# Kernel tuning notes

Measured on AMD Instinct MI355X. Metric: run time of the kernel, lower is better.

The kernel has to match this reference:

```python
import jax, jax.numpy as jnp
import numpy as np

N_HEADS = 4


def setup_inputs() -> dict:
    key = jax.random.key(0)
    ks = jax.random.split(key, 8)
    T, B, V, F = 30, 64, 32, 128   # len_pred, batch, n_vehicles, feature_size
    L, LF, TH = 64, 64, 20         # n_lanes, lane_feature_size, len_hist
    vehicles = jax.random.normal(ks[0], (T, B, V, F), dtype=jnp.float32)
    lanes = jax.random.normal(ks[1], (B, V, L, LF), dtype=jnp.float32)
    mask_lanes = jax.random.randint(ks[2], (TH, B, V, L), 0, 2).astype(bool)
    # torch Linear weight layout [out, in]; conv 1x1 weights squeezed to [out, in]
    Wk = jax.random.normal(ks[3], (F, LF), dtype=jnp.float32) / np.sqrt(LF)
    Wv = jax.random.normal(ks[4], (F, LF), dtype=jnp.float32) / np.sqrt(LF)
    Wq = jax.random.normal(ks[5], (F, F), dtype=jnp.float32) / np.sqrt(F)
    Wc = jax.random.normal(ks[6], (F, F), dtype=jnp.float32) / np.sqrt(F)
    return {"vehicles": vehicles, "lanes": lanes, "mask_lanes": mask_lanes,
            "Wk": Wk, "Wv": Wv, "Wq": Wq, "Wc": Wc}


def reference(vehicles, lanes, mask_lanes, Wk, Wv, Wq, Wc):
    # vehicles: [T,B,V,F], lanes: [B,V,L,LF], mask_lanes: [TH,B,V,L] bool
    T, B, V, F = vehicles.shape
    L = lanes.shape[2]
    H = N_HEADS
    hd = F // H
    # Linear projections of lanes (torch Linear: y = x @ W.T)
    k = jnp.einsum('bvlf,gf->bvlg', lanes, Wk).reshape(B, V, L, H, hd)
    v = jnp.einsum('bvlf,gf->bvlg', lanes, Wv).reshape(B, V, L, H, hd)
    # 1x1 Conv2d on feature channels == per-position linear
    q = jnp.einsum('tbvf,gf->tbvg', vehicles, Wq).reshape(T, B, V, H, hd)
    # mask: any over history dim -> [B,V,L] (the second any in attention is a no-op
    # since the mask is repeated identically over T and heads)
    mask = jnp.any(mask_lanes, axis=0)  # [B,V,L]
    scores = jnp.einsum('tbvhd,bvlhd->tbvhl', q, k) / jnp.sqrt(jnp.float32(hd))
    scores = jnp.where(mask[None, :, :, None, :], scores, jnp.float32(-1e9))
    p = jax.nn.softmax(scores, axis=-1)  # [T,B,V,H,L]
    out = jnp.einsum('tbvhl,bvlhd->tbvhd', p, v).reshape(T, B, V, F)
    out = jnp.einsum('tbvf,gf->tbvg', out, Wc) + vehicles
    return out
```

## Files before the change

### kernel.cpp

```cpp
#include <hip/hip_runtime.h>
#include <hip/hip_bf16.h>

#define T_  30
#define B_  64
#define V_  32
#define F_  128
#define L_  64
#define LF_ 64
#define TH_ 20
#define H_  4
#define HD_ 32

typedef __attribute__((ext_vector_type(8))) short bf16x8;
typedef __attribute__((ext_vector_type(4))) float f32x4;
#define MFMA(a,b,c) __builtin_amdgcn_mfma_f32_16x16x32_bf16(a, b, c, 0, 0, 0)

__device__ __forceinline__ float bf1(unsigned short u) {
    unsigned int x = ((unsigned int)u) << 16; float f; __builtin_memcpy(&f, &x, 4); return f;
}
__device__ __forceinline__ unsigned int cvtpk(float a, float b) {
    __hip_bfloat162 h = __float22bfloat162_rn(make_float2(a, b));
    unsigned int r; __builtin_memcpy(&r, &h, 4); return r;
}
__device__ __forceinline__ void st4pk(unsigned short* p, float a, float b, float c, float d) {
    uint2 u = { cvtpk(a, b), cvtpk(c, d) };
    *(uint2*)p = u;
}
__device__ __forceinline__ bf16x8 ldWfrag(const void* W, int off, bool isBf16) {
    if (isBf16) return *(const bf16x8*)((const unsigned short*)W + off);
    const float* p = (const float*)W + off;
    float4 a = *(const float4*)p;
    float4 b = *(const float4*)(p + 4);
    uint4 u = { cvtpk(a.x, a.y), cvtpk(a.z, a.w), cvtpk(b.x, b.y), cvtpk(b.z, b.w) };
    bf16x8 r; __builtin_memcpy(&r, &u, 16); return r;
}

__global__ __launch_bounds__(512, 4)
void lane_attn_kernel(const void* __restrict__ veh,
                      const void* __restrict__ lanes,
                      const void* __restrict__ maskp,
                      const void* __restrict__ Wk, const void* __restrict__ Wv,
                      const void* __restrict__ Wq, const void* __restrict__ Wc,
                      float* __restrict__ outp)
{
    const int bv    = blockIdx.x;
    const int tid   = threadIdx.x;
    const int w     = tid >> 6;
    const int h     = w >> 1;
    const int shalf = w & 1;
    const int lane  = tid & 63;
    const int quad  = lane >> 4;
    const int lm    = lane & 15;
    const int fbase = h * 32;
    const int fs    = fbase + shalf * 16;

    __shared__ __align__(16) unsigned short sRegion[14336];
    __shared__ __align__(16) unsigned short sK [64 * 136];
    __shared__ __align__(16) unsigned short sVt[128 * 72];
    unsigned short* sQ     = sRegion;
    unsigned short* sO     = sRegion;
    unsigned short* sLanes = sRegion + 4352;
    unsigned short* sVehB  = sRegion + 9984;
    unsigned short* sS     = sRegion + 4352;

    const unsigned short* vh16 = (const unsigned short*)veh;
    const int field = (vh16[2 * lane] >> 7) & 0xFF;
    const bool isBf16 = __popcll(__ballot(field >= 100 && field <= 130)) >= 32;
    const unsigned char* mbp = (const unsigned char*)maskp;
    const bool maskByte = (__ballot(mbp[4 * lane + 1] != 0) != 0ULL);

    bool ok;
    {
        const int* mi = (const int*)maskp;
        int o = 0;
        #pragma unroll
        for (int th = 0; th < TH_; ++th) {
            const size_t e = (size_t)th * (B_ * V_ * L_) + (size_t)bv * L_ + lane;
            o |= maskByte ? (int)mbp[e] : mi[e];
        }
        ok = (o != 0);
    }
    const unsigned long long mok = __ballot(ok);

    bf16x8 wbK[2], wbV[2], wq[4];
    #pragma unroll
    for (int kt = 0; kt < 2; ++kt) {
        const int off = (fs + lm) * 64 + kt * 32 + quad * 8;
        wbK[kt] = ldWfrag(Wk, off, isBf16);
        wbV[kt] = ldWfrag(Wv, off, isBf16);
    }
    #pragma unroll
    for (int kt = 0; kt < 4; ++kt)
        wq[kt] = ldWfrag(Wq, (fs + lm) * 128 + kt * 32 + quad * 8, isBf16);

    for (int u = tid; u < 64 * 16; u += 512) {
        const int l = u >> 4, c4 = u & 15;
        if (isBf16) {
            ushort4 x = ((const ushort4*)lanes)[bv * (L_ * LF_ / 4) + u];
            *(ushort4*)&sLanes[l * 88 + c4 * 4] = x;
        } else {
            float4 x = ((const float4*)lanes)[bv * (L_ * LF_ / 4) + u];
            uint2 y = { cvtpk(x.x, x.y), cvtpk(x.z, x.w) };
            *(uint2*)&sLanes[l * 88 + c4 * 4] = y;
        }
    }
    for (int u = tid; u < 32 * 32; u += 512) {
        const int t = u >> 5, c4 = u & 31;
        uint2 y = { 0, 0 };
        if (t < T_) {
            const int idx = (t * (B_ * V_) + bv) * (F_ / 4) + c4;
            if (isBf16) {
                ushort4 x = ((const ushort4*)veh)[idx];
                __builtin_memcpy(&y, &x, 8);
            } else {
                float4 x = ((const float4*)veh)[idx];
                y.x = cvtpk(x.x, x.y); y.y = cvtpk(x.z, x.w);
            }
        }
        *(uint2*)&sVehB[t * 136 + c4 * 4] = y;
    }
    __syncthreads();

    {
        f32x4 accK[4], accV[4];
        #pragma unroll
        for (int mt = 0; mt < 4; ++mt) { accK[mt] = (f32x4)0.f; accV[mt] = (f32x4)0.f; }
        #pragma unroll
        for (int kt = 0; kt < 2; ++kt) {
            bf16x8 a[4];
            #pragma unroll
            for (int mt = 0; mt < 4; ++mt)
                a[mt] = *(const bf16x8*)&sLanes[(mt * 16 + lm) * 88 + kt * 32 + quad * 8];
            #pragma unroll
            for (int mt = 0; mt < 4; ++mt) {
                accK[mt] = MFMA(wbK[kt], a[mt], accK[mt]);
                accV[mt] = MFMA(a[mt], wbV[kt], accV[mt]);
            }
        }
        #pragma unroll
        for (int mt = 0; mt < 4; ++mt) {
            st4pk(&sK[(mt * 16 + lm) * 136 + fs + quad * 4],
                  accK[mt][0], accK[mt][1], accK[mt][2], accK[mt][3]);
            st4pk(&sVt[(fs + lm) * 72 + mt * 16 + quad * 4],
                  accV[mt][0], accV[mt][1], accV[mt][2], accV[mt][3]);
        }
    }

    {
        f32x4 acc[2];
        acc[0] = (f32x4)0.f; acc[1] = (f32x4)0.f;
        #pragma unroll
        for (int kt = 0; kt < 4; ++kt) {
            bf16x8 b[2];
            #pragma unroll
            for (int nt = 0; nt < 2; ++nt)
                b[nt] = *(const bf16x8*)&sVehB[(nt * 16 + lm) * 136 + kt * 32 + quad * 8];
            #pragma unroll
            for (int nt = 0; nt < 2; ++nt) acc[nt] = MFMA(wq[kt], b[nt], acc[nt]);
        }
        const float sc = 0.17677669529663687f;
        #pragma unroll
        for (int nt = 0; nt < 2; ++nt)
            st4pk(&sQ[(nt * 16 + lm) * 136 + fs + quad * 4],
                  acc[nt][0] * sc, acc[nt][1] * sc, acc[nt][2] * sc, acc[nt][3] * sc);
    }

    bf16x8 wc[4];
    #pragma unroll
    for (int kt = 0; kt < 4; ++kt)
        wc[kt] = ldWfrag(Wc, (fs + lm) * 128 + kt * 32 + quad * 8, isBf16);

    __syncthreads();

    {
        bf16x8 a[4], b;
        #pragma unroll
        for (int mt = 0; mt < 4; ++mt)
            a[mt] = *(const bf16x8*)&sK[(mt * 16 + lm) * 136 + fbase + quad * 8];
        b = *(const bf16x8*)&sQ[(shalf * 16 + lm) * 136 + fbase + quad * 8];
        const int t = shalf * 16 + lm;
        const bool tok = (t < T_);
        const unsigned long long msh = (tok ? mok : 0ULL) >> (quad * 4);
        const unsigned int mlo = (unsigned int)msh, mhi = (unsigned int)(msh >> 32);
        #pragma unroll
        for (int mt = 0; mt < 4; ++mt) {
            f32x4 acc = MFMA(a[mt], b, (f32x4)0.f);
            const unsigned int mw = (mt >= 2) ? mhi : mlo;
            const int bp = (mt * 16) & 31;
            float e0 = ((mw >> (bp + 0)) & 1u) ? __expf(acc[0]) : 0.f;
            float e1 = ((mw >> (bp + 1)) & 1u) ? __expf(acc[1]) : 0.f;
            float e2 = ((mw >> (bp + 2)) & 1u) ? __expf(acc[2]) : 0.f;
            float e3 = ((mw >> (bp + 3)) & 1u) ? __expf(acc[3]) : 0.f;
            uint2 y = { cvtpk(e0, e1), cvtpk(e2, e3) };
            *(uint2*)&sS[(h * 32 + t) * 72 + mt * 16 + quad * 4] = y;
        }
    }

    {
        bf16x8 bones;
        #pragma unroll
        for (int j = 0; j < 8; ++j) bones[j] = (short)0x3F80;
        f32x4 acc[2], ssum;
        acc[0] = (f32x4)0.f; acc[1] = (f32x4)0.f; ssum = (f32x4)0.f;
        #pragma unroll
        for (int kt = 0; kt < 2; ++kt) {
            bf16x8 bp = *(const bf16x8*)&sS[(h * 32 + shalf * 16 + lm) * 72 + kt * 32 + quad * 8];
            bf16x8 av[2];
            #pragma unroll
            for (int mt = 0; mt < 2; ++mt)
                av[mt] = *(const bf16x8*)&sVt[(fbase + mt * 16 + lm) * 72 + kt * 32 + quad * 8];
            ssum = MFMA(bones, bp, ssum);
            #pragma unroll
            for (int mt = 0; mt < 2; ++mt) acc[mt] = MFMA(av[mt], bp, acc[mt]);
        }
        const float sv  = ssum[0];
        const float inv = (sv > 0.f) ? 1.f / sv : 0.f;
        const int t = shalf * 16 + lm;
        #pragma unroll
        for (int mt = 0; mt < 2; ++mt)
            st4pk(&sO[t * 136 + fbase + mt * 16 + quad * 4],
                  acc[mt][0] * inv, acc[mt][1] * inv, acc[mt][2] * inv, acc[mt][3] * inv);
    }

    float4 res[2];
    #pragma unroll
    for (int nt = 0; nt < 2; ++nt) {
        const int t = nt * 16 + lm;
        res[nt] = make_float4(0.f, 0.f, 0.f, 0.f);
        if (t < T_) {
            const size_t off = ((size_t)t * (B_ * V_) + bv) * F_ + fs + quad * 4;
            if (isBf16) {
                ushort4 u = *(const ushort4*)((const unsigned short*)veh + off);
                res[nt] = make_float4(bf1(u.x), bf1(u.y), bf1(u.z), bf1(u.w));
            } else {
                res[nt] = *(const float4*)((const float*)veh + off);
            }
        }
    }
    __syncthreads();

    {
        f32x4 acc[2];
        acc[0] = (f32x4)0.f; acc[1] = (f32x4)0.f;
        #pragma unroll
        for (int kt = 0; kt < 4; ++kt) {
            bf16x8 b[2];
            #pragma unroll
            for (int nt = 0; nt < 2; ++nt)
                b[nt] = *(const bf16x8*)&sO[(nt * 16 + lm) * 136 + kt * 32 + quad * 8];
            #pragma unroll
            for (int nt = 0; nt < 2; ++nt) acc[nt] = MFMA(wc[kt], b[nt], acc[nt]);
        }
        #pragma unroll
        for (int nt = 0; nt < 2; ++nt) {
            const int t = nt * 16 + lm;
            if (t < T_) {
                const size_t off = ((size_t)t * (B_ * V_) + bv) * F_ + fs + quad * 4;
                float4 o = make_float4(acc[nt][0] + res[nt].x, acc[nt][1] + res[nt].y,
                                       acc[nt][2] + res[nt].z, acc[nt][3] + res[nt].w);
                *(float4*)&outp[off] = o;
            }
        }
    }
}

extern "C" void kernel_launch(void* const* d_in, const int* in_sizes, int n_in,
                              void* d_out, int out_size, void* d_ws, size_t ws_size,
                              hipStream_t stream) {
    (void)in_sizes; (void)n_in; (void)out_size; (void)d_ws; (void)ws_size;
    lane_attn_kernel<<<dim3(B_ * V_), dim3(512), 0, stream>>>(
        d_in[0], d_in[1], d_in[2], d_in[3], d_in[4], d_in[5], d_in[6],
        (float*)d_out);
}
```

Baseline: 172.4 us.

## Swizzle LDS layouts, keep V and P in registers, raise occupancy

Replaces padded LDS rows with XOR-swizzled layouts, which shrinks shared memory from about 62KB to 40KB per block. The V projection and the softmax probabilities now stay in registers and feed 16x16x16 MFMAs directly, so the transposed V buffer and the ones-vector sum MFMA are gone. The row sum is computed with wave shuffles, and probabilities are exchanged with the partner wave through a small LDS buffer behind an extra barrier. Launch bounds move to 8 blocks per CU and the Wc load is deferred, both to raise occupancy; the cost is an added sync and register pressure that may cause spills.

```diff
diff --git a/kernel.cpp b/kernel.cpp
--- a/kernel.cpp
+++ b/kernel.cpp
@@ -12,8 +12,17 @@
 #define HD_ 32
 
 typedef __attribute__((ext_vector_type(8))) short bf16x8;
+typedef __attribute__((ext_vector_type(4))) short bf16x4;
 typedef __attribute__((ext_vector_type(4))) float f32x4;
 #define MFMA(a,b,c) __builtin_amdgcn_mfma_f32_16x16x32_bf16(a, b, c, 0, 0, 0)
+
+__device__ __forceinline__ f32x4 mfma16(bf16x4 a, bf16x4 b, f32x4 c) {
+#if defined(__HIP_DEVICE_COMPILE__)
+    return __builtin_amdgcn_mfma_f32_16x16x16bf16_1k(a, b, c, 0, 0, 0);
+#else
+    (void)a; (void)b; return c;
+#endif
+}
 
 __device__ __forceinline__ float bf1(unsigned short u) {
     unsigned int x = ((unsigned int)u) << 16; float f; __builtin_memcpy(&f, &x, 4); return f;
@@ -26,6 +35,8 @@
     uint2 u = { cvtpk(a, b), cvtpk(c, d) };
     *(uint2*)p = u;
 }
+__device__ __forceinline__ int swz128(int r, int c) { return r * 128 + (c ^ ((r & 7) << 3)); }
+__device__ __forceinline__ int swz64 (int r, int c) { return r * 64  + (c ^ ((r & 7) << 3)); }
 __device__ __forceinline__ bf16x8 ldWfrag(const void* W, int off, bool isBf16) {
     if (isBf16) return *(const bf16x8*)((const unsigned short*)W + off);
     const float* p = (const float*)W + off;
@@ -35,7 +46,7 @@
     bf16x8 r; __builtin_memcpy(&r, &u, 16); return r;
 }
 
-__global__ __launch_bounds__(512, 4)
+__global__ __launch_bounds__(512, 8)
 void lane_attn_kernel(const void* __restrict__ veh,
                       const void* __restrict__ lanes,
                       const void* __restrict__ maskp,
@@ -54,14 +65,14 @@
     const int fbase = h * 32;
     const int fs    = fbase + shalf * 16;
 
-    __shared__ __align__(16) unsigned short sRegion[14336];
-    __shared__ __align__(16) unsigned short sK [64 * 136];
-    __shared__ __align__(16) unsigned short sVt[128 * 72];
-    unsigned short* sQ     = sRegion;
-    unsigned short* sO     = sRegion;
-    unsigned short* sLanes = sRegion + 4352;
-    unsigned short* sVehB  = sRegion + 9984;
-    unsigned short* sS     = sRegion + 4352;
+    __shared__ __align__(16) unsigned short sK   [8192];
+    __shared__ __align__(16) unsigned short sReg1[8192];
+    __shared__ __align__(16) unsigned short sReg2[4096];
+    unsigned short* sLanes = sReg1;
+    unsigned short* sVehB  = sReg1 + 4096;
+    unsigned short* sPx    = sReg1;
+    unsigned short* sQ     = sReg2;
+    unsigned short* sO     = sReg2;
 
     const unsigned short* vh16 = (const unsigned short*)veh;
     const int field = (vh16[2 * lane] >> 7) & 0xFF;
@@ -93,56 +104,80 @@
     for (int kt = 0; kt < 4; ++kt)
         wq[kt] = ldWfrag(Wq, (fs + lm) * 128 + kt * 32 + quad * 8, isBf16);
 
-    for (int u = tid; u < 64 * 16; u += 512) {
-        const int l = u >> 4, c4 = u & 15;
-        if (isBf16) {
-            ushort4 x = ((const ushort4*)lanes)[bv * (L_ * LF_ / 4) + u];
-            *(ushort4*)&sLanes[l * 88 + c4 * 4] = x;
-        } else {
-            float4 x = ((const float4*)lanes)[bv * (L_ * LF_ / 4) + u];
+    if (isBf16) {
+        {
+            const int l = tid >> 3, g = tid & 7;
+            uint4 x = *(const uint4*)((const unsigned short*)lanes + (size_t)bv * 4096 + tid * 8);
+            *(uint4*)&sLanes[swz64(l, g * 8)] = x;
+        }
+        {
+            const int t = tid >> 4, g = tid & 15;
+            uint4 x = {0, 0, 0, 0};
+            if (t < T_)
+                x = *(const uint4*)((const unsigned short*)veh + ((size_t)t * (B_ * V_) + bv) * F_ + g * 8);
+            *(uint4*)&sVehB[swz128(t, g * 8)] = x;
+        }
+    } else {
+        const float4* lf4 = (const float4*)lanes;
+        #pragma unroll
+        for (int rr = 0; rr < 2; ++rr) {
+            const int u = tid + rr * 512;
+            const int l = u >> 4, c = (u & 15) * 4;
+            float4 x = lf4[bv * 1024 + u];
             uint2 y = { cvtpk(x.x, x.y), cvtpk(x.z, x.w) };
-            *(uint2*)&sLanes[l * 88 + c4 * 4] = y;
-        }
-    }
-    for (int u = tid; u < 32 * 32; u += 512) {
-        const int t = u >> 5, c4 = u & 31;
-        uint2 y = { 0, 0 };
-        if (t < T_) {
-            const int idx = (t * (B_ * V_) + bv) * (F_ / 4) + c4;
-            if (isBf16) {
-                ushort4 x = ((const ushort4*)veh)[idx];
-                __builtin_memcpy(&y, &x, 8);
-            } else {
-                float4 x = ((const float4*)veh)[idx];
+            *(uint2*)&sLanes[swz64(l, c)] = y;
+        }
+        #pragma unroll
+        for (int rr = 0; rr < 2; ++rr) {
+            const int u = tid + rr * 512;
+            const int t = u >> 5, c = (u & 31) * 4;
+            uint2 y = {0, 0};
+            if (t < T_) {
+                float4 x = ((const float4*)veh)[((size_t)t * (B_ * V_) + bv) * 32 + (u & 31)];
                 y.x = cvtpk(x.x, x.y); y.y = cvtpk(x.z, x.w);
             }
-        }
-        *(uint2*)&sVehB[t * 136 + c4 * 4] = y;
+            *(uint2*)&sVehB[swz128(t, c)] = y;
+        }
     }
     __syncthreads();
 
     {
-        f32x4 accK[4], accV[4];
-        #pragma unroll
-        for (int mt = 0; mt < 4; ++mt) { accK[mt] = (f32x4)0.f; accV[mt] = (f32x4)0.f; }
+        f32x4 accK[4];
+        #pragma unroll
+        for (int mt = 0; mt < 4; ++mt) accK[mt] = (f32x4)0.f;
         #pragma unroll
         for (int kt = 0; kt < 2; ++kt) {
             bf16x8 a[4];
             #pragma unroll
             for (int mt = 0; mt < 4; ++mt)
-                a[mt] = *(const bf16x8*)&sLanes[(mt * 16 + lm) * 88 + kt * 32 + quad * 8];
-            #pragma unroll
-            for (int mt = 0; mt < 4; ++mt) {
-                accK[mt] = MFMA(wbK[kt], a[mt], accK[mt]);
-                accV[mt] = MFMA(a[mt], wbV[kt], accV[mt]);
-            }
+                a[mt] = *(const bf16x8*)&sLanes[swz64(mt * 16 + lm, kt * 32 + quad * 8)];
+            #pragma unroll
+            for (int mt = 0; mt < 4; ++mt) accK[mt] = MFMA(wbK[kt], a[mt], accK[mt]);
+        }
+        #pragma unroll
+        for (int mt = 0; mt < 4; ++mt)
+            st4pk(&sK[swz128(mt * 16 + lm, fs + quad * 4)],
+                  accK[mt][0], accK[mt][1], accK[mt][2], accK[mt][3]);
+    }
+
+    bf16x4 vb[4];
+    {
+        f32x4 accV[4];
+        #pragma unroll
+        for (int mt = 0; mt < 4; ++mt) accV[mt] = (f32x4)0.f;
+        #pragma unroll
+        for (int kt = 0; kt < 2; ++kt) {
+            bf16x8 a[4];
+            #pragma unroll
+            for (int mt = 0; mt < 4; ++mt)
+                a[mt] = *(const bf16x8*)&sLanes[swz64(mt * 16 + lm, kt * 32 + quad * 8)];
+            #pragma unroll
+            for (int mt = 0; mt < 4; ++mt) accV[mt] = MFMA(a[mt], wbV[kt], accV[mt]);
         }
         #pragma unroll
         for (int mt = 0; mt < 4; ++mt) {
-            st4pk(&sK[(mt * 16 + lm) * 136 + fs + quad * 4],
-                  accK[mt][0], accK[mt][1], accK[mt][2], accK[mt][3]);
-            st4pk(&sVt[(fs + lm) * 72 + mt * 16 + quad * 4],
-                  accV[mt][0], accV[mt][1], accV[mt][2], accV[mt][3]);
+            uint2 y = { cvtpk(accV[mt][0], accV[mt][1]), cvtpk(accV[mt][2], accV[mt][3]) };
+            __builtin_memcpy(&vb[mt], &y, 8);
         }
     }
 
@@ -154,72 +189,79 @@
             bf16x8 b[2];
             #pragma unroll
             for (int nt = 0; nt < 2; ++nt)
-                b[nt] = *(const bf16x8*)&sVehB[(nt * 16 + lm) * 136 + kt * 32 + quad * 8];
+                b[nt] = *(const bf16x8*)&sVehB[swz128(nt * 16 + lm, kt * 32 + quad * 8)];
             #pragma unroll
             for (int nt = 0; nt < 2; ++nt) acc[nt] = MFMA(wq[kt], b[nt], acc[nt]);
         }
         const float sc = 0.17677669529663687f;
         #pragma unroll
         for (int nt = 0; nt < 2; ++nt)
-            st4pk(&sQ[(nt * 16 + lm) * 136 + fs + quad * 4],
+            st4pk(&sQ[swz128(nt * 16 + lm, fs + quad * 4)],
                   acc[nt][0] * sc, acc[nt][1] * sc, acc[nt][2] * sc, acc[nt][3] * sc);
     }
-
-    bf16x8 wc[4];
-    #pragma unroll
-    for (int kt = 0; kt < 4; ++kt)
-        wc[kt] = ldWfrag(Wc, (fs + lm) * 128 + kt * 32 + quad * 8, isBf16);
-
     __syncthreads();
 
+    bf16x4 pa[4];
     {
         bf16x8 a[4], b;
         #pragma unroll
         for (int mt = 0; mt < 4; ++mt)
-            a[mt] = *(const bf16x8*)&sK[(mt * 16 + lm) * 136 + fbase + quad * 8];
-        b = *(const bf16x8*)&sQ[(shalf * 16 + lm) * 136 + fbase + quad * 8];
+            a[mt] = *(const bf16x8*)&sK[swz128(mt * 16 + lm, fbase + quad * 8)];
+        b = *(const bf16x8*)&sQ[swz128(shalf * 16 + lm, fbase + quad * 8)];
         const int t = shalf * 16 + lm;
         const bool tok = (t < T_);
         const unsigned long long msh = (tok ? mok : 0ULL) >> (quad * 4);
         const unsigned int mlo = (unsigned int)msh, mhi = (unsigned int)(msh >> 32);
+        float e[4][4];
+        float psum = 0.f;
         #pragma unroll
         for (int mt = 0; mt < 4; ++mt) {
             f32x4 acc = MFMA(a[mt], b, (f32x4)0.f);
             const unsigned int mw = (mt >= 2) ? mhi : mlo;
             const int bp = (mt * 16) & 31;
-            float e0 = ((mw >> (bp + 0)) & 1u) ? __expf(acc[0]) : 0.f;
-            float e1 = ((mw >> (bp + 1)) & 1u) ? __expf(acc[1]) : 0.f;
-            float e2 = ((mw >> (bp + 2)) & 1u) ? __expf(acc[2]) : 0.f;
-            float e3 = ((mw >> (bp + 3)) & 1u) ? __expf(acc[3]) : 0.f;
-            uint2 y = { cvtpk(e0, e1), cvtpk(e2, e3) };
-            *(uint2*)&sS[(h * 32 + t) * 72 + mt * 16 + quad * 4] = y;
-        }
-    }
-
-    {
-        bf16x8 bones;
-        #pragma unroll
-        for (int j = 0; j < 8; ++j) bones[j] = (short)0x3F80;
-        f32x4 acc[2], ssum;
-        acc[0] = (f32x4)0.f; acc[1] = (f32x4)0.f; ssum = (f32x4)0.f;
-        #pragma unroll
-        for (int kt = 0; kt < 2; ++kt) {
-            bf16x8 bp = *(const bf16x8*)&sS[(h * 32 + shalf * 16 + lm) * 72 + kt * 32 + quad * 8];
-            bf16x8 av[2];
-            #pragma unroll
-            for (int mt = 0; mt < 2; ++mt)
-                av[mt] = *(const bf16x8*)&sVt[(fbase + mt * 16 + lm) * 72 + kt * 32 + quad * 8];
-            ssum = MFMA(bones, bp, ssum);
-            #pragma unroll
-            for (int mt = 0; mt < 2; ++mt) acc[mt] = MFMA(av[mt], bp, acc[mt]);
-        }
-        const float sv  = ssum[0];
-        const float inv = (sv > 0.f) ? 1.f / sv : 0.f;
-        const int t = shalf * 16 + lm;
-        #pragma unroll
-        for (int mt = 0; mt < 2; ++mt)
-            st4pk(&sO[t * 136 + fbase + mt * 16 + quad * 4],
-                  acc[mt][0] * inv, acc[mt][1] * inv, acc[mt][2] * inv, acc[mt][3] * inv);
+            #pragma unroll
+            for (int r = 0; r < 4; ++r) {
+                e[mt][r] = ((mw >> (bp + r)) & 1u) ? __expf(acc[r]) : 0.f;
+                psum += e[mt][r];
+            }
+        }
+        psum += __shfl_xor(psum, 16, 64);
+        psum += __shfl_xor(psum, 32, 64);
+        const float inv = (psum > 0.f) ? 1.f / psum : 0.f;
+        #pragma unroll
+        for (int mt = 0; mt < 4; ++mt) {
+            uint2 y = { cvtpk(e[mt][0] * inv, e[mt][1] * inv),
+                        cvtpk(e[mt][2] * inv, e[mt][3] * inv) };
+            __builtin_memcpy(&pa[mt], &y, 8);
+            *(uint2*)&sPx[w * 1024 + swz64(lm, mt * 16 + quad * 4)] = y;
+        }
+    }
+    __syncthreads();
+
+    {
+        bf16x4 pl[4];
+        const unsigned short* sPp = sPx + (w ^ 1) * 1024;
+        #pragma unroll
+        for (int kt = 0; kt < 4; ++kt) {
+            uint2 y = *(const uint2*)&sPp[swz64(lm, kt * 16 + quad * 4)];
+            __builtin_memcpy(&pl[kt], &y, 8);
+        }
+        f32x4 o0 = (f32x4)0.f, o1 = (f32x4)0.f;
+        if (shalf == 0) {
+            #pragma unroll
+            for (int kt = 0; kt < 4; ++kt) {
+                o0 = mfma16(vb[kt], pa[kt], o0);
+                o1 = mfma16(vb[kt], pl[kt], o1);
+            }
+        } else {
+            #pragma unroll
+            for (int kt = 0; kt < 4; ++kt) {
+                o0 = mfma16(vb[kt], pl[kt], o0);
+                o1 = mfma16(vb[kt], pa[kt], o1);
+            }
+        }
+        st4pk(&sO[swz128(lm,      fs + quad * 4)], o0[0], o0[1], o0[2], o0[3]);
+        st4pk(&sO[swz128(16 + lm, fs + quad * 4)], o1[0], o1[1], o1[2], o1[3]);
     }
 
     float4 res[2];
@@ -240,6 +282,10 @@
     __syncthreads();
 
     {
+        bf16x8 wc[4];
+        #pragma unroll
+        for (int kt = 0; kt < 4; ++kt)
+            wc[kt] = ldWfrag(Wc, (fs + lm) * 128 + kt * 32 + quad * 8, isBf16);
         f32x4 acc[2];
         acc[0] = (f32x4)0.f; acc[1] = (f32x4)0.f;
         #pragma unroll
@@ -247,7 +293,7 @@
             bf16x8 b[2];
             #pragma unroll
             for (int nt = 0; nt < 2; ++nt)
-                b[nt] = *(const bf16x8*)&sO[(nt * 16 + lm) * 136 + kt * 32 + quad * 8];
+                b[nt] = *(const bf16x8*)&sO[swz128(nt * 16 + lm, kt * 32 + quad * 8)];
             #pragma unroll
             for (int nt = 0; nt < 2; ++nt) acc[nt] = MFMA(wc[kt], b[nt], acc[nt]);
         }
```

Result: slower. 217.8 us (+26.3%).
